# Optimization experiments

Hardware: AMD Instinct MI355X
Metric: run time of the kernel (lower is better)

Reference implementation:

```python
import jax, jax.numpy as jnp
import numpy as np

# ---- model hyperparameters (match init_kwargs) ----
D_MODEL = 1024
D_STATE = 128
EXPAND = 2
HEADDIM = 64
NGROUPS = 1
D_INNER = EXPAND * D_MODEL            # 2048
NHEADS = D_INNER // HEADDIM           # 32
ROPE_FRAC = 0.5
SPLIT = int(D_STATE * ROPE_FRAC)      # 64 rotary dims
NANG = SPLIT // 2                     # 32 rope angles
A_FLOOR = 1e-4
EPS = 1e-5
BATCH, SEQLEN = 1, 1024
SIZES = [D_INNER, D_INNER, D_STATE * NGROUPS, D_STATE * NGROUPS, NHEADS, NHEADS, NHEADS, NANG]
D_IN_PROJ = int(np.sum(SIZES))        # 4480


def setup_inputs() -> dict:
    key = jax.random.key(0)
    ks = jax.random.split(key, 6)
    u = jax.random.normal(ks[0], (BATCH, SEQLEN, D_MODEL), dtype=jnp.float32)
    W_in = jax.random.normal(ks[1], (D_MODEL, D_IN_PROJ), dtype=jnp.float32) * 0.02
    # dt_bias ~ log(dt) for dt in [1e-3, 0.1] -> around -4
    dt_bias = jax.random.normal(ks[2], (NHEADS,), dtype=jnp.float32) * 0.5 - 4.0
    B_bias = jnp.ones((NHEADS, D_STATE), jnp.float32) + 0.01 * jax.random.normal(ks[3], (NHEADS, D_STATE), dtype=jnp.float32)
    C_bias = jnp.ones((NHEADS, D_STATE), jnp.float32) + 0.01 * jax.random.normal(ks[4], (NHEADS, D_STATE), dtype=jnp.float32)
    Bn_w = jnp.ones((D_STATE,), jnp.float32)
    Cn_w = jnp.ones((D_STATE,), jnp.float32)
    D_param = jnp.ones((NHEADS,), jnp.float32)
    W_out = jax.random.normal(ks[5], (D_INNER, D_MODEL), dtype=jnp.float32) * 0.02
    return {"u": u, "W_in": W_in, "dt_bias": dt_bias, "B_bias": B_bias, "C_bias": C_bias,
            "Bn_w": Bn_w, "Cn_w": Cn_w, "D_param": D_param, "W_out": W_out}


def _rmsnorm(v, w):
    return v * jax.lax.rsqrt(jnp.mean(v * v, axis=-1, keepdims=True) + EPS) * w


def _forward(u, W_in, dt_bias, B_bias, C_bias, Bn_w, Cn_w, D_param, W_out):
    b, l, _ = u.shape
    proj = u @ W_in                                   # (b, l, d_in_proj)
    idx = np.cumsum(SIZES)[:-1]
    z, x, Bp, Cp, dd_dt, dd_A, trap_raw, ang = jnp.split(proj, idx, axis=-1)
    z = z.reshape(b, l, NHEADS, HEADDIM)
    x = x.reshape(b, l, NHEADS, HEADDIM)
    # A = clamp(-softplus(.), max=-A_floor);  dt = softplus(. + dt_bias)
    A = jnp.minimum(-jax.nn.softplus(dd_A), -A_FLOOR)          # (b,l,H)
    dt = jax.nn.softplus(dd_dt + dt_bias)                      # (b,l,H)
    a = jnp.exp(A * dt)                                        # decay per step
    lam = jax.nn.sigmoid(trap_raw)                             # trapezoid gate
    # RMSNorm on B/C (ngroups=1), then per-head additive bias
    Bn = _rmsnorm(Bp, Bn_w)                                    # (b,l,N)
    Cn = _rmsnorm(Cp, Cn_w)
    Bh = Bn[:, :, None, :] + B_bias                            # (b,l,H,N)
    Ch = Cn[:, :, None, :] + C_bias
    # data-dependent rotary: cumulative angle = cumsum(angles * dt)
    theta = jnp.cumsum(ang[:, :, None, :] * dt[..., None], axis=1)  # (b,l,H,NANG)
    cos, sin = jnp.cos(theta), jnp.sin(theta)

    def rope(v):
        d1, d2, rest = v[..., :NANG], v[..., NANG:SPLIT], v[..., SPLIT:]
        return jnp.concatenate([d1 * cos - d2 * sin, d1 * sin + d2 * cos, rest], axis=-1)

    Bh, Ch = rope(Bh), rope(Ch)

    tfirst = lambda v: jnp.moveaxis(v, 1, 0)
    inputs = (tfirst(Bh), tfirst(Ch), tfirst(x), tfirst(a), tfirst(dt), tfirst(lam))
    h0 = jnp.zeros((b, NHEADS, HEADDIM, D_STATE), jnp.float32)
    k0 = jnp.zeros((b, NHEADS, D_STATE), jnp.float32)
    v0 = jnp.zeros((b, NHEADS, HEADDIM), jnp.float32)

    def step(carry, inp):
        h, kp, vp = carry
        Bt, Ct, xt, at, dtt, lamt = inp
        # trapezoidal selective-scan update:
        # h_t = a_t h_{t-1} + dt_t (lam_t B_t x_t + (1-lam_t) a_t B_{t-1} x_{t-1})
        cur = jnp.einsum('bhp,bhn->bhpn', xt, Bt) * (dtt * lamt)[..., None, None]
        prv = jnp.einsum('bhp,bhn->bhpn', vp, kp) * (dtt * (1.0 - lamt) * at)[..., None, None]
        h = at[..., None, None] * h + cur + prv
        yt = jnp.einsum('bhn,bhpn->bhp', Ct, h)
        return (h, Bt, xt), yt

    _, y = jax.lax.scan(step, (h0, k0, v0), inputs)          # (l,b,H,P)
    y = jnp.moveaxis(y, 0, 1) + D_param[None, None, :, None] * x
    y = y * jax.nn.silu(z)                                    # gated output (no out-proj norm)
    return y.reshape(b, l, D_INNER) @ W_out


def reference(u, W_in, dt_bias, B_bias, C_bias, Bn_w, Cn_w, D_param, W_out):
    return _forward(u, W_in, dt_bias, B_bias, C_bias, Bn_w, Cn_w, D_param, W_out)
```

## Files before the change

kernel.cpp:

```cpp
#include <hip/hip_runtime.h>
#include <stdint.h>

#define SEQ     1024

typedef __attribute__((ext_vector_type(8))) short short8;
typedef __attribute__((ext_vector_type(4))) float f4;

__device__ __forceinline__ short f2b(float f){
  union { float f; uint32_t u; } v; v.f = f;
  uint32_t r = (v.u + 0x7fffu + ((v.u >> 16) & 1u)) >> 16;
  return (short)(uint16_t)r;
}
__device__ __forceinline__ float b2f(uint16_t u){
  union { uint32_t u; float f; } v; v.u = ((uint32_t)u) << 16; return v.f;
}
__device__ __forceinline__ uint32_t pack2(float lo, float hi){
  return (uint32_t)(uint16_t)f2b(lo) | ((uint32_t)(uint16_t)f2b(hi) << 16);
}
__device__ __forceinline__ float softplus_f(float x){
  return x > 20.f ? x : log1pf(__expf(x));
}
__device__ __forceinline__ void gload_lds16(const short* g, short* l){
  __builtin_amdgcn_global_load_lds((const __attribute__((address_space(1))) void*)g,
                                   (__attribute__((address_space(3))) void*)l, 16, 0, 0);
}

__global__ __launch_bounds__(256) void prep_inputs(const float* __restrict__ u, short* __restrict__ u16,
                                                   const float* __restrict__ W_in, short* __restrict__ WtIn,
                                                   const float* __restrict__ W_out, short* __restrict__ WtOut,
                                                   float* __restrict__ outz){
  int b = blockIdx.x;
  int tid = threadIdx.x;
  if (b < 1024){
    int i = (b * 256 + tid) * 4;
    f4 v = *(const f4*)(u + i);
    uint2 pk; pk.x = pack2(v.x, v.y); pk.y = pack2(v.z, v.w);
    *(uint2*)(u16 + i) = pk;
    return;
  }
  if (b >= 2656){
    int i = ((b - 2656) * 256 + tid) * 4;
    *(f4*)(outz + i) = (f4){0.f, 0.f, 0.f, 0.f};
    return;
  }
  const float* in; short* outp; int R, lda, bx, by;
  if (b < 2144){ int idx = b - 1024; bx = idx % 140; by = idx / 140; in = W_in;  outp = WtIn;  R = 1024; lda = 4480; }
  else         { int idx = b - 2144; bx = idx & 31;  by = idx >> 5;  in = W_out; outp = WtOut; R = 2048; lda = 1024; }
  __shared__ float tile[32][132];
  int bc = bx * 32, br = by * 128;
  int c = tid & 31, r0 = tid >> 5;
  #pragma unroll
  for (int i = 0; i < 16; i++){
    int r = r0 + i * 8;
    tile[c][r] = in[(size_t)(br + r) * lda + bc + c];
  }
  __syncthreads();
  #pragma unroll
  for (int i = 0; i < 4; i++){
    int task = tid + 256 * i;
    int cc = task >> 5;
    int rg = (task & 31) * 4;
    f4 v = *(const f4*)&tile[cc][rg];
    uint2 pk; pk.x = pack2(v.x, v.y); pk.y = pack2(v.z, v.w);
    *(uint2*)(outp + (size_t)(bc + cc) * R + br + rg) = pk;
  }
}

__global__ __launch_bounds__(256) void gemm1_kernel(const short* __restrict__ A, const short* __restrict__ Bt,
                                                    short* __restrict__ zx, short* __restrict__ xTb,
                                                    float* __restrict__ projT){
  const int K = 1024;
  __shared__ __align__(16) short As[3][64 * 64];
  __shared__ __align__(16) short Bs[3][128 * 64];
  const int tid  = threadIdx.x;
  const int wave = tid >> 6;
  const int lane = tid & 63;
  const int m0 = blockIdx.y * 64;
  const int n0 = blockIdx.x * 128;
  const int wm = (wave >> 1) * 32;
  const int wn = (wave & 1) * 64;
  const int quad = lane >> 4;
  const int r16  = lane & 15;
  const int rsw  = r16 & 7;

  f4 acc[2][4];
  #pragma unroll
  for (int i = 0; i < 2; i++)
    #pragma unroll
    for (int j = 0; j < 4; j++) acc[i][j] = (f4){0.f, 0.f, 0.f, 0.f};

  const int srow = tid >> 3;
  const int soct = tid & 7;
  const int og   = (soct ^ (srow & 7)) * 8;
  const short* gA0 = A  + (size_t)(m0 + srow) * K + og;
  const short* gB0 = Bt + (size_t)(n0 + srow) * K + og;

#define G1_STAGE(buf, kt) do {                                              \
    const int ko_ = (kt) * 64;                                              \
    gload_lds16(gA0 + ko_,                   &As[buf][tid * 8]);            \
    gload_lds16(gA0 + (size_t)32 * K + ko_,  &As[buf][tid * 8 + 2048]);     \
    gload_lds16(gB0 + ko_,                   &Bs[buf][tid * 8]);            \
    gload_lds16(gB0 + (size_t)32 * K + ko_,  &Bs[buf][tid * 8 + 2048]);     \
    gload_lds16(gB0 + (size_t)64 * K + ko_,  &Bs[buf][tid * 8 + 4096]);     \
    gload_lds16(gB0 + (size_t)96 * K + ko_,  &Bs[buf][tid * 8 + 6144]);     \
  } while(0)

  G1_STAGE(0, 0);
  G1_STAGE(1, 1);

  for (int kt = 0; kt < 16; ++kt){
    if (kt < 15) asm volatile("s_waitcnt vmcnt(6)" ::: "memory");
    else         asm volatile("s_waitcnt vmcnt(0)" ::: "memory");
    __builtin_amdgcn_s_barrier();
    __builtin_amdgcn_sched_barrier(0);
    if (kt + 2 < 16){
      int nb = kt + 2 - ((kt + 2) / 3) * 3;
      G1_STAGE(nb, kt + 2);
    }
    const short* Ac = As[kt % 3];
    const short* Bc = Bs[kt % 3];
    #pragma unroll
    for (int ks = 0; ks < 2; ++ks){
      const int oq = ((ks * 4 + quad) ^ rsw) * 8;
      short8 af[2], bf[4];
      #pragma unroll
      for (int i = 0; i < 2; i++)
        af[i] = *(const short8*)&Ac[(wm + i * 16 + r16) * 64 + oq];
      #pragma unroll
      for (int j = 0; j < 4; j++)
        bf[j] = *(const short8*)&Bc[(wn + j * 16 + r16) * 64 + oq];
      #pragma unroll
      for (int i = 0; i < 2; i++)
        #pragma unroll
        for (int j = 0; j < 4; j++)
          acc[i][j] = __builtin_amdgcn_mfma_f32_16x16x32_bf16(af[i], bf[j], acc[i][j], 0, 0, 0);
    }
  }
#undef G1_STAGE

  #pragma unroll
  for (int i = 0; i < 2; i++)
    #pragma unroll
    for (int j = 0; j < 4; j++){
      int colb = n0 + wn + j * 16 + r16;
      int rowb = m0 + wm + i * 16 + quad * 4;
      if (colb < 2048){
        #pragma unroll
        for (int rr = 0; rr < 4; ++rr)
          zx[(size_t)(rowb + rr) * 4096 + colb] = f2b(acc[i][j][rr]);
      } else if (colb < 4096){
        uint2 pk; pk.x = pack2(acc[i][j][0], acc[i][j][1]); pk.y = pack2(acc[i][j][2], acc[i][j][3]);
        *(uint2*)(xTb + (size_t)(colb - 2048) * 1024 + rowb) = pk;
        #pragma unroll
        for (int rr = 0; rr < 4; ++rr)
          zx[(size_t)(rowb + rr) * 4096 + colb] = f2b(acc[i][j][rr]);
      } else {
        #pragma unroll
        for (int rr = 0; rr < 4; ++rr)
          projT[(size_t)(rowb + rr) * 384 + (colb - 4096)] = acc[i][j][rr];
      }
    }
}

__global__ __launch_bounds__(256) void gemm2_kernel(const short* __restrict__ A, const short* __restrict__ Bt,
                                                    float* __restrict__ C){
  const int N = 1024, K = 2048;
  __shared__ __align__(16) short As[3][64 * 64];
  __shared__ __align__(16) short Bs[3][128 * 64];
  const int tid  = threadIdx.x;
  const int wave = tid >> 6;
  const int lane = tid & 63;
  const int m0 = blockIdx.y * 64;
  const int n0 = blockIdx.x * 128;
  const int k0 = blockIdx.z * 512;
  const int wm = (wave >> 1) * 32;
  const int wn = (wave & 1) * 64;
  const int quad = lane >> 4;
  const int r16  = lane & 15;
  const int rsw  = r16 & 7;

  f4 acc[2][4];
  #pragma unroll
  for (int i = 0; i < 2; i++)
    #pragma unroll
    for (int j = 0; j < 4; j++) acc[i][j] = (f4){0.f, 0.f, 0.f, 0.f};

  const int srow = tid >> 3;
  const int soct = tid & 7;
  const int og   = (soct ^ (srow & 7)) * 8;
  const short* gA0 = A  + (size_t)(m0 + srow) * K + k0 + og;
  const short* gB0 = Bt + (size_t)(n0 + srow) * K + k0 + og;

#define G2_STAGE(buf, kt) do {                                              \
    const int ko_ = (kt) * 64;                                              \
    gload_lds16(gA0 + ko_,                   &As[buf][tid * 8]);            \
    gload_lds16(gA0 + (size_t)32 * K + ko_,  &As[buf][tid * 8 + 2048]);     \
    gload_lds16(gB0 + ko_,                   &Bs[buf][tid * 8]);            \
    gload_lds16(gB0 + (size_t)32 * K + ko_,  &Bs[buf][tid * 8 + 2048]);     \
    gload_lds16(gB0 + (size_t)64 * K + ko_,  &Bs[buf][tid * 8 + 4096]);     \
    gload_lds16(gB0 + (size_t)96 * K + ko_,  &Bs[buf][tid * 8 + 6144]);     \
  } while(0)

  G2_STAGE(0, 0);
  G2_STAGE(1, 1);

  for (int kt = 0; kt < 8; ++kt){
    if (kt < 7) asm volatile("s_waitcnt vmcnt(6)" ::: "memory");
    else        asm volatile("s_waitcnt vmcnt(0)" ::: "memory");
    __builtin_amdgcn_s_barrier();
    __builtin_amdgcn_sched_barrier(0);
    if (kt + 2 < 8){
      int nb = kt + 2 - ((kt + 2) / 3) * 3;
      G2_STAGE(nb, kt + 2);
    }
    const short* Ac = As[kt % 3];
    const short* Bc = Bs[kt % 3];
    #pragma unroll
    for (int ks = 0; ks < 2; ++ks){
      const int oq = ((ks * 4 + quad) ^ rsw) * 8;
      short8 af[2], bf[4];
      #pragma unroll
      for (int i = 0; i < 2; i++)
        af[i] = *(const short8*)&Ac[(wm + i * 16 + r16) * 64 + oq];
      #pragma unroll
      for (int j = 0; j < 4; j++)
        bf[j] = *(const short8*)&Bc[(wn + j * 16 + r16) * 64 + oq];
      #pragma unroll
      for (int i = 0; i < 2; i++)
        #pragma unroll
        for (int j = 0; j < 4; j++)
          acc[i][j] = __builtin_amdgcn_mfma_f32_16x16x32_bf16(af[i], bf[j], acc[i][j], 0, 0, 0);
    }
  }
#undef G2_STAGE

  #pragma unroll
  for (int i = 0; i < 2; i++)
    #pragma unroll
    for (int j = 0; j < 4; j++)
      #pragma unroll
      for (int rr = 0; rr < 4; ++rr){
        int row = m0 + wm + i * 16 + quad * 4 + rr;
        int col = n0 + wn + j * 16 + r16;
        unsafeAtomicAdd(&C[(size_t)row * N + col], acc[i][j][rr]);
      }
}

__global__ __launch_bounds__(256) void scan_theta(const float* __restrict__ projT,
                                                  const float* __restrict__ dt_bias,
                                                  float* __restrict__ Lcum, float* __restrict__ u2b,
                                                  float* __restrict__ c1b,
                                                  float* __restrict__ cosb, float* __restrict__ sinb){
  int b = blockIdx.x;
  int tid = threadIdx.x;
  int t0 = tid * 4;
  int lane = tid & 63, wave = tid >> 6;
  __shared__ float wsum[4];
  if (b < 32){
    int h = b;
    float dtbias = dt_bias[h];
    float dt5[5], lam5[5];
    #pragma unroll
    for (int i = 0; i < 5; i++){
      int t = t0 + i;
      if (t < 1024){
        const float* row = projT + (size_t)t * 384;
        dt5[i]  = softplus_f(row[256 + h] + dtbias);
        lam5[i] = 1.f / (1.f + __expf(-row[320 + h]));
      } else { dt5[i] = 0.f; lam5[i] = 0.f; }
    }
    float v[4], c1[4], c2n[4];
    #pragma unroll
    for (int i = 0; i < 4; i++){
      int t = t0 + i;
      const float* row = projT + (size_t)t * 384;
      float Ah = -fmaxf(softplus_f(row[288 + h]), 1e-4f);
      v[i]   = Ah * dt5[i];
      c1[i]  = dt5[i] * lam5[i];
      c2n[i] = dt5[i + 1] * (1.f - lam5[i + 1]);
    }
    v[1] += v[0]; v[2] += v[1]; v[3] += v[2];
    float tot = v[3], sc = tot;
    #pragma unroll
    for (int off = 1; off < 64; off <<= 1){
      float n = __shfl_up(sc, off, 64);
      if (lane >= off) sc += n;
    }
    if (lane == 63) wsum[wave] = sc;
    __syncthreads();
    float base = sc - tot;
    for (int w = 0; w < wave; ++w) base += wsum[w];
    #pragma unroll
    for (int i = 0; i < 4; i++){
      int t = t0 + i;
      Lcum[h * 1024 + t] = base + v[i];
      u2b[h * 1024 + t]  = c1[i] + c2n[i];
      c1b[h * 1024 + t]  = c1[i];
    }
  } else {
    int hk = b - 32;
    int h = hk >> 5, k = hk & 31;
    float dtbias = dt_bias[h];
    float v[4];
    #pragma unroll
    for (int i = 0; i < 4; i++){
      const float* row = projT + (size_t)(t0 + i) * 384;
      float dt = softplus_f(row[256 + h] + dtbias);
      v[i] = row[352 + k] * dt;
    }
    v[1] += v[0]; v[2] += v[1]; v[3] += v[2];
    float tot = v[3], sc = tot;
    #pragma unroll
    for (int off = 1; off < 64; off <<= 1){
      float n = __shfl_up(sc, off, 64);
      if (lane >= off) sc += n;
    }
    if (lane == 63) wsum[wave] = sc;
    __syncthreads();
    float base = sc - tot;
    for (int w = 0; w < wave; ++w) base += wsum[w];
    #pragma unroll
    for (int i = 0; i < 4; i++){
      float th = base + v[i];
      float s, c;
      __sincosf(th, &s, &c);
      int t = t0 + i;
      cosb[(size_t)t * 1024 + h * 32 + k] = c;
      sinb[(size_t)t * 1024 + h * 32 + k] = s;
    }
  }
}

__global__ __launch_bounds__(256) void bcxt_kernel(const float* __restrict__ projT,
                                                   const float* __restrict__ B_bias, const float* __restrict__ C_bias,
                                                   const float* __restrict__ Bn_w, const float* __restrict__ Cn_w,
                                                   const float* __restrict__ cosb, const float* __restrict__ sinb,
                                                   short* __restrict__ Bb, short* __restrict__ Cb){
  int t = blockIdx.x;
  int tid = threadIdx.x;
  __shared__ float vv[2][128];
  __shared__ float red[4];
  int n = tid & 127;
  int isC = tid >> 7;
  float val = projT[(size_t)t * 384 + isC * 128 + n];
  float ss = val * val;
  #pragma unroll
  for (int off = 32; off >= 1; off >>= 1) ss += __shfl_down(ss, off);
  int wave = tid >> 6, lane = tid & 63;
  if (lane == 0) red[wave] = ss;
  __syncthreads();
  float rsv = isC ? rsqrtf((red[2] + red[3]) * (1.f / 128.f) + 1e-5f)
                  : rsqrtf((red[0] + red[1]) * (1.f / 128.f) + 1e-5f);
  vv[isC][n] = val * rsv * (isC ? Cn_w[n] : Bn_w[n]);
  __syncthreads();
  const float* cb = cosb + (size_t)t * 1024;
  const float* sb = sinb + (size_t)t * 1024;
  #pragma unroll
  for (int it = 0; it < 8; it++){
    int task = tid + 256 * it;
    int arr  = task >> 10;
    int rem  = task & 1023;
    int h    = rem >> 5;
    int n0   = (rem & 31) * 4;
    const float* bias = arr ? C_bias : B_bias;
    const float* base = vv[arr];
    f4 bv = *(const f4*)&base[n0];
    f4 bi = *(const f4*)&bias[h * 128 + n0];
    f4 o;
    if (n0 < 32){
      f4 bv2 = *(const f4*)&base[n0 + 32];
      f4 bi2 = *(const f4*)&bias[h * 128 + n0 + 32];
      f4 cv = *(const f4*)&cb[h * 32 + n0];
      f4 sv = *(const f4*)&sb[h * 32 + n0];
      #pragma unroll
      for (int q = 0; q < 4; q++) o[q] = (bv[q] + bi[q]) * cv[q] - (bv2[q] + bi2[q]) * sv[q];
    } else if (n0 < 64){
      int k0 = n0 - 32;
      f4 bv1 = *(const f4*)&base[k0];
      f4 bi1 = *(const f4*)&bias[h * 128 + k0];
      f4 cv = *(const f4*)&cb[h * 32 + k0];
      f4 sv = *(const f4*)&sb[h * 32 + k0];
      #pragma unroll
      for (int q = 0; q < 4; q++) o[q] = (bv1[q] + bi1[q]) * sv[q] + (bv[q] + bi[q]) * cv[q];
    } else {
      #pragma unroll
      for (int q = 0; q < 4; q++) o[q] = bv[q] + bi[q];
    }
    uint2 pk; pk.x = pack2(o.x, o.y); pk.y = pack2(o.z, o.w);
    short* outp = arr ? Cb : Bb;
    *(uint2*)(outp + (size_t)t * 4096 + h * 128 + n0) = pk;
  }
}

__global__ __launch_bounds__(256) void hpart_kernel(const short* __restrict__ xTb, const short* __restrict__ Bb,
                                                    const float* __restrict__ Lcum, const float* __restrict__ u2b,
                                                    short* __restrict__ Hpart){
  int h = blockIdx.x >> 4, c = (blockIdx.x >> 1) & 7, nh = blockIdx.x & 1;
  int t0 = c * 128;
  int tid = threadIdx.x;
  __shared__ float wS[128];
  if (tid < 128){
    float Lend = Lcum[h * 1024 + t0 + 127];
    wS[tid] = __expf(Lend - Lcum[h * 1024 + t0 + tid]) * u2b[h * 1024 + t0 + tid];
  }
  __syncthreads();
  int wave = tid >> 6, lane = tid & 63, quad = lane >> 4, r16 = lane & 15;
  int n0 = nh * 64 + wave * 16;
  f4 acc[4];
  #pragma unroll
  for (int i = 0; i < 4; i++) acc[i] = (f4){0.f, 0.f, 0.f, 0.f};

  const ushort* Bh = (const ushort*)Bb + (size_t)t0 * 4096 + h * 128;
  #pragma unroll
  for (int kk = 0; kk < 4; ++kk){
    int sb = kk * 32 + quad * 8;
    short8 af[4];
    #pragma unroll
    for (int i = 0; i < 4; i++){
      int p = i * 16 + r16;
      af[i] = *(const short8*)(xTb + (size_t)(h * 64 + p) * 1024 + t0 + sb);
    }
    float wv[8];
    #pragma unroll
    for (int jj = 0; jj < 8; jj++) wv[jj] = wS[sb + jj];
    int nn = n0 + r16;
    float e[8];
    #pragma unroll
    for (int jj = 0; jj < 8; jj++)
      e[jj] = b2f(Bh[(size_t)(sb + jj) * 4096 + nn]) * wv[jj];
    union { short8 s; uint32_t u[4]; } fr;
    #pragma unroll
    for (int q = 0; q < 4; q++) fr.u[q] = pack2(e[2 * q], e[2 * q + 1]);
    short8 bfr = fr.s;
    #pragma unroll
    for (int i = 0; i < 4; i++)
      acc[i] = __builtin_amdgcn_mfma_f32_16x16x32_bf16(af[i], bfr, acc[i], 0, 0, 0);
  }

  short* out = Hpart + ((size_t)(h * 8 + c)) * 8192;
  int nn = n0 + r16;
  #pragma unroll
  for (int i = 0; i < 4; i++)
    #pragma unroll
    for (int rr = 0; rr < 4; ++rr){
      int p = i * 16 + quad * 4 + rr;
      out[p * 128 + nn] = f2b(acc[i][rr]);
    }
}

#define GS 144
__global__ __launch_bounds__(256) void chunky_kernel(const short* __restrict__ Cb, const short* __restrict__ Bbg,
                                                     const short* __restrict__ xTb, const short* __restrict__ Hpart,
                                                     const float* __restrict__ Lcum, const float* __restrict__ u2b,
                                                     const float* __restrict__ c1b,
                                                     const short* __restrict__ zx, const float* __restrict__ D_par,
                                                     short* __restrict__ yb16){
  int h = blockIdx.x >> 4, c = (blockIdx.x >> 1) & 7, half = blockIdx.x & 1;
  int t0 = c * 128;
  int tb = half * 64;
  __shared__ __align__(16) short Gt[64 * GS];
  __shared__ __align__(16) short Hu[64 * 128];
  __shared__ float Lc[128], u2v[128], c1v[128];
  int tid = threadIdx.x;
  if (tid < 128){
    Lc[tid]  = Lcum[h * 1024 + t0 + tid];
    u2v[tid] = u2b[h * 1024 + t0 + tid];
    c1v[tid] = c1b[h * 1024 + t0 + tid];
  }
  float Lprev = (c > 0) ? Lcum[h * 1024 + t0 - 1] : 0.f;
  float Dp = D_par[h];

  {
    float hacc[32];
    #pragma unroll
    for (int q = 0; q < 32; q++) hacc[q] = 0.f;
    for (int cp = 0; cp < c; ++cp){
      float dec = __expf(Lprev - Lcum[h * 1024 + cp * 128 + 127]);
      const short8* hp = (const short8*)((const ushort*)Hpart + ((size_t)(h * 8 + cp)) * 8192 + tid * 32);
      #pragma unroll
      for (int q = 0; q < 4; q++){
        short8 v = hp[q];
        #pragma unroll
        for (int e = 0; e < 8; e++) hacc[q * 8 + e] += dec * b2f((uint16_t)v[e]);
      }
    }
    int p = tid >> 2;
    int wbase = tid * 64;
    #pragma unroll
    for (int q = 0; q < 4; q++){
      union { short8 s; uint32_t u[4]; } fr;
      #pragma unroll
      for (int p2 = 0; p2 < 4; p2++) fr.u[p2] = pack2(hacc[q * 8 + p2 * 2], hacc[q * 8 + p2 * 2 + 1]);
      int off = (wbase + q * 16) ^ ((p & 7) << 4);
      *(short8*)((char*)Hu + off) = fr.s;
    }
  }

  int wave = tid >> 6, lane = tid & 63, quad = lane >> 4, r16 = lane & 15;
  int wm2 = (wave >> 1) * 32, wn2 = (wave & 1) * 64;

  f4 acc[2][4];
  #pragma unroll
  for (int i = 0; i < 2; i++)
    #pragma unroll
    for (int j = 0; j < 4; j++) acc[i][j] = (f4){0.f, 0.f, 0.f, 0.f};
  #pragma unroll
  for (int kk = 0; kk < 4; ++kk){
    short8 af[2], bf[4];
    #pragma unroll
    for (int i = 0; i < 2; i++)
      af[i] = *(const short8*)(Cb + (size_t)(t0 + tb + wm2 + i * 16 + r16) * 4096 + h * 128 + kk * 32 + quad * 8);
    #pragma unroll
    for (int j = 0; j < 4; j++)
      bf[j] = *(const short8*)(Bbg + (size_t)(t0 + wn2 + j * 16 + r16) * 4096 + h * 128 + kk * 32 + quad * 8);
    #pragma unroll
    for (int i = 0; i < 2; i++)
      #pragma unroll
      for (int j = 0; j < 4; j++)
        acc[i][j] = __builtin_amdgcn_mfma_f32_16x16x32_bf16(af[i], bf[j], acc[i][j], 0, 0, 0);
  }
  __syncthreads();

  #pragma unroll
  for (int i = 0; i < 2; i++){
    #pragma unroll
    for (int rr = 0; rr < 4; ++rr){
      int tl = wm2 + i * 16 + quad * 4 + rr;
      int trow = tb + tl;
      float Lt = Lc[trow];
      #pragma unroll
      for (int j = 0; j < 4; j++){
        int scol = wn2 + j * 16 + r16;
        float g = 0.f;
        if (scol <= trow){
          float wcoef = (scol == trow) ? c1v[scol] : u2v[scol];
          g = acc[i][j][rr] * wcoef * __expf(Lt - Lc[scol]);
        }
        Gt[tl * GS + scol] = f2b(g);
      }
    }
  }
  __syncthreads();

  f4 accY[4], accZ[4];
  #pragma unroll
  for (int j = 0; j < 4; j++){ accY[j] = (f4){0.f,0.f,0.f,0.f}; accZ[j] = (f4){0.f,0.f,0.f,0.f}; }
  int m0 = wave * 16;
  #pragma unroll
  for (int kk = 0; kk < 4; ++kk){
    short8 ag, ac, bx[4], bh[4];
    ag = *(const short8*)&Gt[(m0 + r16) * GS + kk * 32 + quad * 8];
    ac = *(const short8*)(Cb + (size_t)(t0 + tb + m0 + r16) * 4096 + h * 128 + kk * 32 + quad * 8);
    #pragma unroll
    for (int j = 0; j < 4; j++){
      bx[j] = *(const short8*)(xTb + (size_t)(h * 64 + j * 16 + r16) * 1024 + t0 + kk * 32 + quad * 8);
      int hrow = j * 16 + r16;
      int hoff = (hrow * 256 + kk * 64 + quad * 16) ^ ((hrow & 7) << 4);
      bh[j] = *(const short8*)((const char*)Hu + hoff);
    }
    #pragma unroll
    for (int j = 0; j < 4; j++){
      accY[j] = __builtin_amdgcn_mfma_f32_16x16x32_bf16(ag, bx[j], accY[j], 0, 0, 0);
      accZ[j] = __builtin_amdgcn_mfma_f32_16x16x32_bf16(ac, bh[j], accZ[j], 0, 0, 0);
    }
  }
  const ushort* zxu = (const ushort*)zx;
  #pragma unroll
  for (int rr = 0; rr < 4; ++rr){
    int tl = m0 + quad * 4 + rr;
    int trow = tb + tl;
    float ei = __expf(Lc[trow] - Lprev);
    const ushort* zrow = zxu + (size_t)(t0 + trow) * 4096;
    #pragma unroll
    for (int j = 0; j < 4; j++){
      int col = h * 64 + j * 16 + r16;
      float zv = b2f(zrow[col]);
      float xv = b2f(zrow[2048 + col]);
      float yv = accY[j][rr] + ei * accZ[j][rr] + Dp * xv;
      float o = yv * (zv / (1.f + __expf(-zv)));
      yb16[(size_t)(t0 + trow) * 2048 + col] = f2b(o);
    }
  }
}

extern "C" void kernel_launch(void* const* d_in, const int* in_sizes, int n_in,
                              void* d_out, int out_size, void* d_ws, size_t ws_size,
                              hipStream_t stream){
  const float* u       = (const float*)d_in[0];
  const float* W_in    = (const float*)d_in[1];
  const float* dt_bias = (const float*)d_in[2];
  const float* B_bias  = (const float*)d_in[3];
  const float* C_bias  = (const float*)d_in[4];
  const float* Bn_w    = (const float*)d_in[5];
  const float* Cn_w    = (const float*)d_in[6];
  const float* D_par   = (const float*)d_in[7];
  const float* W_out   = (const float*)d_in[8];
  float* out = (float*)d_out;

  char* ws = (char*)d_ws;
  short* u16   = (short*)(ws + 0);
  short* WtIn  = (short*)(ws + 2097152);
  short* WtOut = (short*)(ws + 11272192);
  short* zx    = (short*)(ws + 15466496);
  float* projT = (float*)(ws + 23855104);
  float* cosb  = (float*)(ws + 25427968);
  float* sinb  = (float*)(ws + 29622272);
  short* Bb    = (short*)(ws + 33816576);
  short* Cb    = (short*)(ws + 42205184);
  short* xTb   = (short*)(ws + 50593792);
  float* Lcum  = (float*)(ws + 54788096);
  float* u2b   = (float*)(ws + 54919168);
  float* c1b   = (float*)(ws + 55050240);
  short* Hpart = (short*)(ws + 55181312);
  short* yb16  = (short*)(ws + 59375616);

  prep_inputs<<<3680, 256, 0, stream>>>(u, u16, W_in, WtIn, W_out, WtOut, out);
  gemm1_kernel<<<dim3(35, 16), 256, 0, stream>>>(u16, WtIn, zx, xTb, projT);
  scan_theta<<<1056, 256, 0, stream>>>(projT, dt_bias, Lcum, u2b, c1b, cosb, sinb);
  bcxt_kernel<<<1024, 256, 0, stream>>>(projT, B_bias, C_bias, Bn_w, Cn_w, cosb, sinb, Bb, Cb);
  hpart_kernel<<<512, 256, 0, stream>>>(xTb, Bb, Lcum, u2b, Hpart);
  chunky_kernel<<<512, 256, 0, stream>>>(Cb, Bb, xTb, Hpart, Lcum, u2b, c1b, zx, D_par, yb16);
  gemm2_kernel<<<dim3(8, 16, 4), 256, 0, stream>>>(yb16, WtOut, out);
}
```

Measured before the change: 201.7 us.

## Load GEMM fragments directly from global memory and remap blocks for XCD locality

Both projection GEMMs stop staging tiles through LDS with a triple-buffered global_load_lds pipeline and barriers. Each wave now reads its MFMA operand fragments straight from global memory into registers. The grids are also flattened to 1D with a remap that spreads consecutive block IDs across the 8 XCDs so that blocks on the same die share A/B tiles in L2. The aim is to cut LDS traffic and barrier overhead. The cost is that operand reuse now depends on the caches instead of LDS, and the software prefetch pipeline is gone.

```diff
diff --git a/kernel.cpp b/kernel.cpp
--- a/kernel.cpp
+++ b/kernel.cpp
@@ -19,10 +19,6 @@
 }
 __device__ __forceinline__ float softplus_f(float x){
   return x > 20.f ? x : log1pf(__expf(x));
-}
-__device__ __forceinline__ void gload_lds16(const short* g, short* l){
-  __builtin_amdgcn_global_load_lds((const __attribute__((address_space(1))) void*)g,
-                                   (__attribute__((address_space(3))) void*)l, 16, 0, 0);
 }
 
 __global__ __launch_bounds__(256) void prep_inputs(const float* __restrict__ u, short* __restrict__ u16,
@@ -70,18 +66,16 @@
                                                     short* __restrict__ zx, short* __restrict__ xTb,
                                                     float* __restrict__ projT){
   const int K = 1024;
-  __shared__ __align__(16) short As[3][64 * 64];
-  __shared__ __align__(16) short Bs[3][128 * 64];
   const int tid  = threadIdx.x;
   const int wave = tid >> 6;
   const int lane = tid & 63;
-  const int m0 = blockIdx.y * 64;
-  const int n0 = blockIdx.x * 128;
+  int wg = (blockIdx.x & 7) * 70 + (blockIdx.x >> 3);
+  const int m0 = (wg & 15) * 64;
+  const int n0 = (wg >> 4) * 128;
   const int wm = (wave >> 1) * 32;
   const int wn = (wave & 1) * 64;
   const int quad = lane >> 4;
   const int r16  = lane & 15;
-  const int rsw  = r16 & 7;
 
   f4 acc[2][4];
   #pragma unroll
@@ -89,54 +83,29 @@
     #pragma unroll
     for (int j = 0; j < 4; j++) acc[i][j] = (f4){0.f, 0.f, 0.f, 0.f};
 
-  const int srow = tid >> 3;
-  const int soct = tid & 7;
-  const int og   = (soct ^ (srow & 7)) * 8;
-  const short* gA0 = A  + (size_t)(m0 + srow) * K + og;
-  const short* gB0 = Bt + (size_t)(n0 + srow) * K + og;
-
-#define G1_STAGE(buf, kt) do {                                              \
-    const int ko_ = (kt) * 64;                                              \
-    gload_lds16(gA0 + ko_,                   &As[buf][tid * 8]);            \
-    gload_lds16(gA0 + (size_t)32 * K + ko_,  &As[buf][tid * 8 + 2048]);     \
-    gload_lds16(gB0 + ko_,                   &Bs[buf][tid * 8]);            \
-    gload_lds16(gB0 + (size_t)32 * K + ko_,  &Bs[buf][tid * 8 + 2048]);     \
-    gload_lds16(gB0 + (size_t)64 * K + ko_,  &Bs[buf][tid * 8 + 4096]);     \
-    gload_lds16(gB0 + (size_t)96 * K + ko_,  &Bs[buf][tid * 8 + 6144]);     \
-  } while(0)
-
-  G1_STAGE(0, 0);
-  G1_STAGE(1, 1);
-
-  for (int kt = 0; kt < 16; ++kt){
-    if (kt < 15) asm volatile("s_waitcnt vmcnt(6)" ::: "memory");
-    else         asm volatile("s_waitcnt vmcnt(0)" ::: "memory");
-    __builtin_amdgcn_s_barrier();
-    __builtin_amdgcn_sched_barrier(0);
-    if (kt + 2 < 16){
-      int nb = kt + 2 - ((kt + 2) / 3) * 3;
-      G1_STAGE(nb, kt + 2);
-    }
-    const short* Ac = As[kt % 3];
-    const short* Bc = Bs[kt % 3];
-    #pragma unroll
-    for (int ks = 0; ks < 2; ++ks){
-      const int oq = ((ks * 4 + quad) ^ rsw) * 8;
-      short8 af[2], bf[4];
-      #pragma unroll
-      for (int i = 0; i < 2; i++)
-        af[i] = *(const short8*)&Ac[(wm + i * 16 + r16) * 64 + oq];
+  const short* pa0 = A  + (size_t)(m0 + wm + r16) * K + quad * 8;
+  const short* pa1 = pa0 + (size_t)16 * K;
+  const short* pb0 = Bt + (size_t)(n0 + wn + r16) * K + quad * 8;
+  const short* pb1 = pb0 + (size_t)16 * K;
+  const short* pb2 = pb0 + (size_t)32 * K;
+  const short* pb3 = pb0 + (size_t)48 * K;
+
+  #pragma unroll 4
+  for (int kt = 0; kt < 32; ++kt){
+    const int ko = kt * 32;
+    short8 af[2], bf[4];
+    af[0] = *(const short8*)(pa0 + ko);
+    af[1] = *(const short8*)(pa1 + ko);
+    bf[0] = *(const short8*)(pb0 + ko);
+    bf[1] = *(const short8*)(pb1 + ko);
+    bf[2] = *(const short8*)(pb2 + ko);
+    bf[3] = *(const short8*)(pb3 + ko);
+    #pragma unroll
+    for (int i = 0; i < 2; i++)
       #pragma unroll
       for (int j = 0; j < 4; j++)
-        bf[j] = *(const short8*)&Bc[(wn + j * 16 + r16) * 64 + oq];
-      #pragma unroll
-      for (int i = 0; i < 2; i++)
-        #pragma unroll
-        for (int j = 0; j < 4; j++)
-          acc[i][j] = __builtin_amdgcn_mfma_f32_16x16x32_bf16(af[i], bf[j], acc[i][j], 0, 0, 0);
-    }
-  }
-#undef G1_STAGE
+        acc[i][j] = __builtin_amdgcn_mfma_f32_16x16x32_bf16(af[i], bf[j], acc[i][j], 0, 0, 0);
+  }
 
   #pragma unroll
   for (int i = 0; i < 2; i++)
@@ -165,19 +134,17 @@
 __global__ __launch_bounds__(256) void gemm2_kernel(const short* __restrict__ A, const short* __restrict__ Bt,
                                                     float* __restrict__ C){
   const int N = 1024, K = 2048;
-  __shared__ __align__(16) short As[3][64 * 64];
-  __shared__ __align__(16) short Bs[3][128 * 64];
   const int tid  = threadIdx.x;
   const int wave = tid >> 6;
   const int lane = tid & 63;
-  const int m0 = blockIdx.y * 64;
-  const int n0 = blockIdx.x * 128;
-  const int k0 = blockIdx.z * 512;
+  int wg = (blockIdx.x & 7) * 64 + (blockIdx.x >> 3);
+  const int m0 = (wg & 15) * 64;
+  const int n0 = ((wg >> 4) & 7) * 128;
+  const int k0 = (wg >> 7) * 512;
   const int wm = (wave >> 1) * 32;
   const int wn = (wave & 1) * 64;
   const int quad = lane >> 4;
   const int r16  = lane & 15;
-  const int rsw  = r16 & 7;
 
   f4 acc[2][4];
   #pragma unroll
@@ -185,54 +152,29 @@
     #pragma unroll
     for (int j = 0; j < 4; j++) acc[i][j] = (f4){0.f, 0.f, 0.f, 0.f};
 
-  const int srow = tid >> 3;
-  const int soct = tid & 7;
-  const int og   = (soct ^ (srow & 7)) * 8;
-  const short* gA0 = A  + (size_t)(m0 + srow) * K + k0 + og;
-  const short* gB0 = Bt + (size_t)(n0 + srow) * K + k0 + og;
-
-#define G2_STAGE(buf, kt) do {                                              \
-    const int ko_ = (kt) * 64;                                              \
-    gload_lds16(gA0 + ko_,                   &As[buf][tid * 8]);            \
-    gload_lds16(gA0 + (size_t)32 * K + ko_,  &As[buf][tid * 8 + 2048]);     \
-    gload_lds16(gB0 + ko_,                   &Bs[buf][tid * 8]);            \
-    gload_lds16(gB0 + (size_t)32 * K + ko_,  &Bs[buf][tid * 8 + 2048]);     \
-    gload_lds16(gB0 + (size_t)64 * K + ko_,  &Bs[buf][tid * 8 + 4096]);     \
-    gload_lds16(gB0 + (size_t)96 * K + ko_,  &Bs[buf][tid * 8 + 6144]);     \
-  } while(0)
-
-  G2_STAGE(0, 0);
-  G2_STAGE(1, 1);
-
-  for (int kt = 0; kt < 8; ++kt){
-    if (kt < 7) asm volatile("s_waitcnt vmcnt(6)" ::: "memory");
-    else        asm volatile("s_waitcnt vmcnt(0)" ::: "memory");
-    __builtin_amdgcn_s_barrier();
-    __builtin_amdgcn_sched_barrier(0);
-    if (kt + 2 < 8){
-      int nb = kt + 2 - ((kt + 2) / 3) * 3;
-      G2_STAGE(nb, kt + 2);
-    }
-    const short* Ac = As[kt % 3];
-    const short* Bc = Bs[kt % 3];
-    #pragma unroll
-    for (int ks = 0; ks < 2; ++ks){
-      const int oq = ((ks * 4 + quad) ^ rsw) * 8;
-      short8 af[2], bf[4];
-      #pragma unroll
-      for (int i = 0; i < 2; i++)
-        af[i] = *(const short8*)&Ac[(wm + i * 16 + r16) * 64 + oq];
+  const short* pa0 = A  + (size_t)(m0 + wm + r16) * K + k0 + quad * 8;
+  const short* pa1 = pa0 + (size_t)16 * K;
+  const short* pb0 = Bt + (size_t)(n0 + wn + r16) * K + k0 + quad * 8;
+  const short* pb1 = pb0 + (size_t)16 * K;
+  const short* pb2 = pb0 + (size_t)32 * K;
+  const short* pb3 = pb0 + (size_t)48 * K;
+
+  #pragma unroll 4
+  for (int kt = 0; kt < 16; ++kt){
+    const int ko = kt * 32;
+    short8 af[2], bf[4];
+    af[0] = *(const short8*)(pa0 + ko);
+    af[1] = *(const short8*)(pa1 + ko);
+    bf[0] = *(const short8*)(pb0 + ko);
+    bf[1] = *(const short8*)(pb1 + ko);
+    bf[2] = *(const short8*)(pb2 + ko);
+    bf[3] = *(const short8*)(pb3 + ko);
+    #pragma unroll
+    for (int i = 0; i < 2; i++)
       #pragma unroll
       for (int j = 0; j < 4; j++)
-        bf[j] = *(const short8*)&Bc[(wn + j * 16 + r16) * 64 + oq];
-      #pragma unroll
-      for (int i = 0; i < 2; i++)
-        #pragma unroll
-        for (int j = 0; j < 4; j++)
-          acc[i][j] = __builtin_amdgcn_mfma_f32_16x16x32_bf16(af[i], bf[j], acc[i][j], 0, 0, 0);
-    }
-  }
-#undef G2_STAGE
+        acc[i][j] = __builtin_amdgcn_mfma_f32_16x16x32_bf16(af[i], bf[j], acc[i][j], 0, 0, 0);
+  }
 
   #pragma unroll
   for (int i = 0; i < 2; i++)
@@ -615,10 +557,10 @@
   short* yb16  = (short*)(ws + 59375616);
 
   prep_inputs<<<3680, 256, 0, stream>>>(u, u16, W_in, WtIn, W_out, WtOut, out);
-  gemm1_kernel<<<dim3(35, 16), 256, 0, stream>>>(u16, WtIn, zx, xTb, projT);
+  gemm1_kernel<<<560, 256, 0, stream>>>(u16, WtIn, zx, xTb, projT);
   scan_theta<<<1056, 256, 0, stream>>>(projT, dt_bias, Lcum, u2b, c1b, cosb, sinb);
   bcxt_kernel<<<1024, 256, 0, stream>>>(projT, B_bias, C_bias, Bn_w, Cn_w, cosb, sinb, Bb, Cb);
   hpart_kernel<<<512, 256, 0, stream>>>(xTb, Bb, Lcum, u2b, Hpart);
   chunky_kernel<<<512, 256, 0, stream>>>(Cb, Bb, xTb, Hpart, Lcum, u2b, c1b, zx, D_par, yb16);
-  gemm2_kernel<<<dim3(8, 16, 4), 256, 0, stream>>>(yb16, WtOut, out);
-}
+  gemm2_kernel<<<512, 256, 0, stream>>>(yb16, WtOut, out);
+}
```

After: 257.4 us. 1.28x slower.
